# Performance work log

Hardware: AMD Instinct MI355X
Metric: run time of the kernel (lower is better)

## Reference

```python
import jax, jax.numpy as jnp
import numpy as np

N_NODES = 100000
N_EDGES = 3200000
IN_F, HID_F, OUT_F = 128, 64, 32
NEG_SLOPE = 0.2


def setup_inputs() -> dict:
    key = jax.random.key(0)
    ks = jax.random.split(key, 10)
    glorot = lambda k, shape: jax.random.normal(k, shape, jnp.float32) * jnp.sqrt(2.0 / (shape[0] + shape[-1]))
    x = jax.random.normal(ks[0], (N_NODES, IN_F), jnp.float32)
    edge_index = jax.random.randint(ks[1], (2, N_EDGES), 0, N_NODES, jnp.int64)
    return {
        "x": x,
        "edge_index": edge_index,
        "W1": glorot(ks[2], (IN_F, HID_F)),
        "att_src1": glorot(ks[3], (HID_F,)),
        "att_dst1": glorot(ks[4], (HID_F,)),
        "b1": jnp.zeros((HID_F,), jnp.float32),
        "W2": glorot(ks[5], (HID_F, OUT_F)),
        "att_src2": glorot(ks[6], (OUT_F,)),
        "att_dst2": glorot(ks[7], (OUT_F,)),
        "b2": jnp.zeros((OUT_F,), jnp.float32),
    }


def _segment_softmax(logits, seg, num_segments):
    m = jax.ops.segment_max(logits, seg, num_segments=num_segments)
    e = jnp.exp(logits - m[seg])
    s = jax.ops.segment_sum(e, seg, num_segments=num_segments)
    return e / s[seg]


def _gat_conv(x, src, dst, W, a_src, a_dst, b, n):
    h = x @ W                                    # [N, F]
    logits = jax.nn.leaky_relu((h @ a_src)[src] + (h @ a_dst)[dst], NEG_SLOPE)  # [E]
    att = _segment_softmax(logits, dst, n)       # softmax over incoming edges per dst
    out = jax.ops.segment_sum(h[src] * att[:, None], dst, num_segments=n)
    return out + b


def reference(x, edge_index, W1, att_src1, att_dst1, b1, W2, att_src2, att_dst2, b2):
    n = x.shape[0]
    loops = jnp.arange(n, dtype=edge_index.dtype)
    src = jnp.concatenate([edge_index[0], loops])  # PyG GATConv adds self-loops
    dst = jnp.concatenate([edge_index[1], loops])
    h = _gat_conv(x, src, dst, W1, att_src1, att_dst1, b1, n)
    h = jax.nn.relu(h)
    h = _gat_conv(h, src, dst, W2, att_src2, att_dst2, b2, n)
    return jax.nn.softmax(h, axis=1)
```

## Files before the change

### kernel.cpp

```cpp
#include <hip/hip_runtime.h>
#include <hip/hip_fp16.h>

#define N_NODES 100000
#define N_EDGES 3200000
#define ET (N_EDGES + N_NODES)
#define IN_F 128
#define HID_F 64
#define OUT_F 32
#define NEG_SLOPE 0.2f

#define NB 391
#define CHUNK_A 8192
#define BLOCKS_A ((ET + CHUNK_A - 1) / CHUNK_A)
#define BKT_CAP 12288
#define HIST_BLOCKS 400


__global__ __launch_bounds__(256) void histB_kernel(const int* __restrict__ ei,
                                                    int* __restrict__ bpart) {
    __shared__ int lh[NB];
    for (int i = threadIdx.x; i < NB; i += 256) lh[i] = 0;
    __syncthreads();
    int stride = HIST_BLOCKS * 256;
    for (int e = blockIdx.x * 256 + threadIdx.x; e < N_EDGES; e += stride) {
        int dst = ei[N_EDGES + e];
        atomicAdd(&lh[dst >> 8], 1);
    }
    __syncthreads();
    for (int i = threadIdx.x; i < NB; i += 256)
        bpart[blockIdx.x * NB + i] = lh[i];
}


__global__ __launch_bounds__(512) void scanB_kernel(const int* __restrict__ bpart,
                                                    int* __restrict__ bucket_base,
                                                    int* __restrict__ gcursor,
                                                    int* __restrict__ row_ptr) {
    __shared__ int a[NB];
    int t = threadIdx.x;
    int cnt = 0;
    if (t < NB) {
        int v = 0;
        for (int c = 0; c < HIST_BLOCKS; ++c) v += bpart[c * NB + t];
        cnt = v + min(256, N_NODES - (t << 8));
        a[t] = cnt;
    }
    __syncthreads();
    for (int off = 1; off < NB; off <<= 1) {
        int v = 0;
        if (t < NB && t >= off) v = a[t - off];
        __syncthreads();
        if (t < NB) a[t] += v;
        __syncthreads();
    }
    if (t < NB) {
        int base = a[t] - cnt;
        bucket_base[t] = base;
        gcursor[t] = base;
    }
    if (t == 0) { bucket_base[NB] = ET; row_ptr[N_NODES] = ET; }
}


__global__ __launch_bounds__(256) void partA_kernel(const int* __restrict__ ei,
                                                    int* __restrict__ gcursor,
                                                    unsigned* __restrict__ staging) {
    __shared__ int cnt[NB];
    __shared__ int inc[NB];
    __shared__ int delta[NB];
    __shared__ unsigned stg[CHUNK_A];
    __shared__ unsigned short bkt[CHUNK_A];
    int t = threadIdx.x;
    int begin = blockIdx.x * CHUNK_A;
    int n = min(CHUNK_A, ET - begin);

    for (int i = t; i < NB; i += 256) cnt[i] = 0;
    __syncthreads();

    for (int i = t; i < n; i += 256) {
        int e = begin + i;
        int dst = (e < N_EDGES) ? ei[N_EDGES + e] : (e - N_EDGES);
        atomicAdd(&cnt[dst >> 8], 1);
    }
    __syncthreads();

    for (int i = t; i < NB; i += 256) inc[i] = cnt[i];
    __syncthreads();
    for (int off = 1; off < NB; off <<= 1) {
        int i0 = t, i1 = t + 256;
        int v0 = (i0 < NB && i0 >= off) ? inc[i0 - off] : 0;
        int v1 = (i1 < NB && i1 >= off) ? inc[i1 - off] : 0;
        __syncthreads();
        if (i0 < NB) inc[i0] += v0;
        if (i1 < NB) inc[i1] += v1;
        __syncthreads();
    }

    for (int i = t; i < NB; i += 256) {
        int c = cnt[i];
        int ls = inc[i] - c;
        int g = (c > 0) ? atomicAdd(&gcursor[i], c) : 0;
        delta[i] = g - ls;
        cnt[i] = ls;
    }
    __syncthreads();

    for (int i = t; i < n; i += 256) {
        int e = begin + i;
        int src, dst;
        if (e < N_EDGES) { src = ei[e]; dst = ei[N_EDGES + e]; }
        else             { src = dst = e - N_EDGES; }
        int b = dst >> 8;
        int pos = atomicAdd(&cnt[b], 1);
        stg[pos] = ((unsigned)(dst & 255) << 17) | (unsigned)src;
        bkt[pos] = (unsigned short)b;
    }
    __syncthreads();

    for (int i = t; i < n; i += 256) {
        staging[delta[bkt[i]] + i] = stg[i];
    }
}


__global__ __launch_bounds__(256) void partB_kernel(const unsigned* __restrict__ staging,
                                                    const int* __restrict__ bucket_base,
                                                    int* __restrict__ row_ptr,
                                                    int* __restrict__ src_sorted) {
    __shared__ int out_s[BKT_CAP];
    __shared__ int a[256];
    __shared__ int cur[256];
    int b = blockIdx.x, t = threadIdx.x;
    int nb0 = b << 8;
    int nn = min(256, N_NODES - nb0);
    int g0 = bucket_base[b];
    int g1 = bucket_base[b + 1];
    int n = g1 - g0;

    cur[t] = 0;
    __syncthreads();
    for (int i = t; i < n; i += 256)
        atomicAdd(&cur[staging[g0 + i] >> 17], 1);
    __syncthreads();

    int v = cur[t];
    a[t] = v;
    __syncthreads();
    for (int off = 1; off < 256; off <<= 1) {
        int w = (t >= off) ? a[t - off] : 0;
        __syncthreads();
        a[t] += w;
        __syncthreads();
    }
    int pref = a[t] - v;
    cur[t] = pref;
    if (t < nn) row_ptr[nb0 + t] = g0 + pref;
    __syncthreads();

    for (int i = t; i < n; i += 256) {
        unsigned u = staging[g0 + i];
        int pos = atomicAdd(&cur[u >> 17], 1);
        out_s[pos] = (int)(u & 0x1FFFFu);
    }
    __syncthreads();
    for (int i = t; i < n; i += 256)
        src_sorted[g0 + i] = out_s[i];
}


__global__ __launch_bounds__(256) void gemm1_kernel(const float* __restrict__ x,
                                                    const float* __restrict__ W,
                                                    const float* __restrict__ a_src,
                                                    const float* __restrict__ a_dst,
                                                    __half* __restrict__ h,
                                                    float* __restrict__ as,
                                                    float* __restrict__ ad) {
    __shared__ float Wl[IN_F * HID_F];
    __shared__ float Xl[64 * 132];
    int t = threadIdx.x;
    int base = blockIdx.x * 64;

    for (int i = t; i < IN_F * HID_F / 4; i += 256)
        ((float4*)Wl)[i] = ((const float4*)W)[i];
#pragma unroll
    for (int i = 0; i < 8; ++i) {
        int f4 = t + 256 * i;
        int r = f4 >> 5, c4 = f4 & 31;
        int gr = base + r; if (gr >= N_NODES) gr = N_NODES - 1;
        ((float4*)Xl)[r * 33 + c4] = ((const float4*)(x + (size_t)gr * IN_F))[c4];
    }
    __syncthreads();

    int tx = t & 15, ty = t >> 4;
    int col = tx * 4, row0 = ty * 4;

    float4 acc0 = {0,0,0,0}, acc1 = {0,0,0,0}, acc2 = {0,0,0,0}, acc3 = {0,0,0,0};

#pragma unroll 4
    for (int k = 0; k < IN_F; k += 4) {
        float4 xv0 = *(const float4*)&Xl[(row0 + 0) * 132 + k];
        float4 xv1 = *(const float4*)&Xl[(row0 + 1) * 132 + k];
        float4 xv2 = *(const float4*)&Xl[(row0 + 2) * 132 + k];
        float4 xv3 = *(const float4*)&Xl[(row0 + 3) * 132 + k];
        float4 wv0 = *(const float4*)&Wl[(k + 0) * HID_F + col];
        float4 wv1 = *(const float4*)&Wl[(k + 1) * HID_F + col];
        float4 wv2 = *(const float4*)&Wl[(k + 2) * HID_F + col];
        float4 wv3 = *(const float4*)&Wl[(k + 3) * HID_F + col];
#define G1STEP(A, XV) \
        A.x = fmaf(XV.x, wv0.x, A.x); A.y = fmaf(XV.x, wv0.y, A.y); \
        A.z = fmaf(XV.x, wv0.z, A.z); A.w = fmaf(XV.x, wv0.w, A.w); \
        A.x = fmaf(XV.y, wv1.x, A.x); A.y = fmaf(XV.y, wv1.y, A.y); \
        A.z = fmaf(XV.y, wv1.z, A.z); A.w = fmaf(XV.y, wv1.w, A.w); \
        A.x = fmaf(XV.z, wv2.x, A.x); A.y = fmaf(XV.z, wv2.y, A.y); \
        A.z = fmaf(XV.z, wv2.z, A.z); A.w = fmaf(XV.z, wv2.w, A.w); \
        A.x = fmaf(XV.w, wv3.x, A.x); A.y = fmaf(XV.w, wv3.y, A.y); \
        A.z = fmaf(XV.w, wv3.z, A.z); A.w = fmaf(XV.w, wv3.w, A.w);
        G1STEP(acc0, xv0) G1STEP(acc1, xv1) G1STEP(acc2, xv2) G1STEP(acc3, xv3)
#undef G1STEP
    }

    float4 av = *(const float4*)&a_src[col];
    float4 dv = *(const float4*)&a_dst[col];
#define G1OUT(I, A) { \
        int grow = base + row0 + I; \
        float vs = A.x*av.x + A.y*av.y + A.z*av.z + A.w*av.w; \
        float vd = A.x*dv.x + A.y*dv.y + A.z*dv.z + A.w*dv.w; \
        vs += __shfl_xor(vs, 1, 64); vd += __shfl_xor(vd, 1, 64); \
        vs += __shfl_xor(vs, 2, 64); vd += __shfl_xor(vd, 2, 64); \
        vs += __shfl_xor(vs, 4, 64); vd += __shfl_xor(vd, 4, 64); \
        vs += __shfl_xor(vs, 8, 64); vd += __shfl_xor(vd, 8, 64); \
        if (grow < N_NODES) { \
            __half2 p0 = __floats2half2_rn(A.x, A.y); \
            __half2 p1 = __floats2half2_rn(A.z, A.w); \
            __half2* hp = (__half2*)&h[(size_t)grow * HID_F + col]; \
            hp[0] = p0; hp[1] = p1; \
            if (tx == 0) { as[grow] = vs; ad[grow] = vd; } \
        } }
    G1OUT(0, acc0) G1OUT(1, acc1) G1OUT(2, acc2) G1OUT(3, acc3)
#undef G1OUT
}


__global__ __launch_bounds__(256) void agg1_kernel(const __half* __restrict__ h,
                                                   const float* __restrict__ as,
                                                   const float* __restrict__ ad,
                                                   const int* __restrict__ row_ptr,
                                                   const int* __restrict__ src_sorted,
                                                   const float* __restrict__ b,
                                                   float* __restrict__ r1) {
    int n = blockIdx.x * 4 + (threadIdx.x >> 6);
    int lane = threadIdx.x & 63;
    if (n >= N_NODES) return;
    int beg = row_ptr[n], end = row_ptr[n + 1];
    int deg = end - beg;
    float adn = ad[n];

    int e0 = beg + lane;
    int sidx = 0;
    float p = 0.f;
    if (e0 < end) {
        sidx = src_sorted[e0];
        float t = as[sidx] + adn;
        t = (t >= 0.f) ? t : NEG_SLOPE * t;
        p = __expf(t);
    }
    float s = p;

    int g  = lane >> 3;
    int ho = (lane & 7) * 8;

    float4 aL = {0,0,0,0}, aH = {0,0,0,0};
#define ACC1(V, W) { \
        float2 f0 = __half22float2(*(const __half2*)&V.x); \
        float2 f1 = __half22float2(*(const __half2*)&V.y); \
        float2 f2 = __half22float2(*(const __half2*)&V.z); \
        float2 f3 = __half22float2(*(const __half2*)&V.w); \
        aL.x = fmaf(f0.x, W, aL.x); aL.y = fmaf(f0.y, W, aL.y); \
        aL.z = fmaf(f1.x, W, aL.z); aL.w = fmaf(f1.y, W, aL.w); \
        aH.x = fmaf(f2.x, W, aH.x); aH.y = fmaf(f2.y, W, aH.y); \
        aH.z = fmaf(f3.x, W, aH.z); aH.w = fmaf(f3.y, W, aH.w); }

#define BATCH1(K0) { \
        float ws0 = __shfl(p, (K0 + 0) * 8 + g, 64); \
        float ws1 = __shfl(p, (K0 + 1) * 8 + g, 64); \
        float ws2 = __shfl(p, (K0 + 2) * 8 + g, 64); \
        float ws3 = __shfl(p, (K0 + 3) * 8 + g, 64); \
        int   ss0 = __shfl(sidx, (K0 + 0) * 8 + g, 64); \
        int   ss1 = __shfl(sidx, (K0 + 1) * 8 + g, 64); \
        int   ss2 = __shfl(sidx, (K0 + 2) * 8 + g, 64); \
        int   ss3 = __shfl(sidx, (K0 + 3) * 8 + g, 64); \
        uint4 v0 = *(const uint4*)&h[(size_t)ss0 * HID_F + ho]; \
        uint4 v1 = *(const uint4*)&h[(size_t)ss1 * HID_F + ho]; \
        uint4 v2 = *(const uint4*)&h[(size_t)ss2 * HID_F + ho]; \
        uint4 v3 = *(const uint4*)&h[(size_t)ss3 * HID_F + ho]; \
        ACC1(v0, ws0) ACC1(v1, ws1) ACC1(v2, ws2) ACC1(v3, ws3) }

    BATCH1(0)
    if (deg > 32) BATCH1(4)
#undef BATCH1

    for (int cb = beg + 64; cb < end; cb += 64) {
        int e = cb + lane;
        float pr = 0.f;
        int sr = 0;
        if (e < end) {
            sr = src_sorted[e];
            float t = as[sr] + adn;
            t = (t >= 0.f) ? t : NEG_SLOPE * t;
            pr = __expf(t);
            s += pr;
        }
        int cnt = min(64, end - cb);
        int rr = (cnt + 7) >> 3;
        for (int k = 0; k < rr; ++k) {
            float wk = __shfl(pr, k * 8 + g, 64);
            int   sk = __shfl(sr, k * 8 + g, 64);
            uint4 hv = *(const uint4*)&h[(size_t)sk * HID_F + ho];
            ACC1(hv, wk)
        }
    }
#undef ACC1

    s += __shfl_xor(s, 32, 64); s += __shfl_xor(s, 16, 64); s += __shfl_xor(s, 8, 64);
    s += __shfl_xor(s, 4, 64);  s += __shfl_xor(s, 2, 64);  s += __shfl_xor(s, 1, 64);
    float invs = __builtin_amdgcn_rcpf(s);

#define RED1(C) C += __shfl_xor(C, 8, 64); C += __shfl_xor(C, 16, 64); C += __shfl_xor(C, 32, 64);
    RED1(aL.x) RED1(aL.y) RED1(aL.z) RED1(aL.w)
    RED1(aH.x) RED1(aH.y) RED1(aH.z) RED1(aH.w)
#undef RED1

    if (lane < 8) {
        int fo = lane * 8;
        float4 b0 = *(const float4*)&b[fo];
        float4 b1 = *(const float4*)&b[fo + 4];
        float4 vL, vH;
        vL.x = fmaxf(fmaf(aL.x, invs, b0.x), 0.f); vL.y = fmaxf(fmaf(aL.y, invs, b0.y), 0.f);
        vL.z = fmaxf(fmaf(aL.z, invs, b0.z), 0.f); vL.w = fmaxf(fmaf(aL.w, invs, b0.w), 0.f);
        vH.x = fmaxf(fmaf(aH.x, invs, b1.x), 0.f); vH.y = fmaxf(fmaf(aH.y, invs, b1.y), 0.f);
        vH.z = fmaxf(fmaf(aH.z, invs, b1.z), 0.f); vH.w = fmaxf(fmaf(aH.w, invs, b1.w), 0.f);
        *(float4*)&r1[(size_t)n * HID_F + fo] = vL;
        *(float4*)&r1[(size_t)n * HID_F + fo + 4] = vH;
    }
}


__global__ __launch_bounds__(256) void gemm2_kernel(const float* __restrict__ r1,
                                                    const float* __restrict__ W,
                                                    const float* __restrict__ a_src,
                                                    const float* __restrict__ a_dst,
                                                    __half* __restrict__ h2,
                                                    float* __restrict__ as2,
                                                    float* __restrict__ ad2) {
    __shared__ float Wl[HID_F * OUT_F];
    __shared__ float Xl[128 * 68];
    int t = threadIdx.x;
    int base = blockIdx.x * 128;

    for (int i = t; i < HID_F * OUT_F / 4; i += 256)
        ((float4*)Wl)[i] = ((const float4*)W)[i];
#pragma unroll
    for (int i = 0; i < 8; ++i) {
        int f4 = t + 256 * i;
        int r = f4 >> 4, c4 = f4 & 15;
        int gr = base + r; if (gr >= N_NODES) gr = N_NODES - 1;
        ((float4*)Xl)[r * 17 + c4] = ((const float4*)(r1 + (size_t)gr * HID_F))[c4];
    }
    __syncthreads();

    int tx = t & 7, ty = t >> 3;
    int col = tx * 4, row0 = ty * 4;

    float4 acc0 = {0,0,0,0}, acc1 = {0,0,0,0}, acc2 = {0,0,0,0}, acc3 = {0,0,0,0};

#pragma unroll 4
    for (int k = 0; k < HID_F; k += 4) {
        float4 xv0 = *(const float4*)&Xl[(row0 + 0) * 68 + k];
        float4 xv1 = *(const float4*)&Xl[(row0 + 1) * 68 + k];
        float4 xv2 = *(const float4*)&Xl[(row0 + 2) * 68 + k];
        float4 xv3 = *(const float4*)&Xl[(row0 + 3) * 68 + k];
        float4 wv0 = *(const float4*)&Wl[(k + 0) * OUT_F + col];
        float4 wv1 = *(const float4*)&Wl[(k + 1) * OUT_F + col];
        float4 wv2 = *(const float4*)&Wl[(k + 2) * OUT_F + col];
        float4 wv3 = *(const float4*)&Wl[(k + 3) * OUT_F + col];
#define G2STEP(A, XV) \
        A.x = fmaf(XV.x, wv0.x, A.x); A.y = fmaf(XV.x, wv0.y, A.y); \
        A.z = fmaf(XV.x, wv0.z, A.z); A.w = fmaf(XV.x, wv0.w, A.w); \
        A.x = fmaf(XV.y, wv1.x, A.x); A.y = fmaf(XV.y, wv1.y, A.y); \
        A.z = fmaf(XV.y, wv1.z, A.z); A.w = fmaf(XV.y, wv1.w, A.w); \
        A.x = fmaf(XV.z, wv2.x, A.x); A.y = fmaf(XV.z, wv2.y, A.y); \
        A.z = fmaf(XV.z, wv2.z, A.z); A.w = fmaf(XV.z, wv2.w, A.w); \
        A.x = fmaf(XV.w, wv3.x, A.x); A.y = fmaf(XV.w, wv3.y, A.y); \
        A.z = fmaf(XV.w, wv3.z, A.z); A.w = fmaf(XV.w, wv3.w, A.w);
        G2STEP(acc0, xv0) G2STEP(acc1, xv1) G2STEP(acc2, xv2) G2STEP(acc3, xv3)
#undef G2STEP
    }

    float4 av = *(const float4*)&a_src[col];
    float4 dv = *(const float4*)&a_dst[col];
#define G2OUT(I, A) { \
        int grow = base + row0 + I; \
        float vs = A.x*av.x + A.y*av.y + A.z*av.z + A.w*av.w; \
        float vd = A.x*dv.x + A.y*dv.y + A.z*dv.z + A.w*dv.w; \
        vs += __shfl_xor(vs, 1, 64); vd += __shfl_xor(vd, 1, 64); \
        vs += __shfl_xor(vs, 2, 64); vd += __shfl_xor(vd, 2, 64); \
        vs += __shfl_xor(vs, 4, 64); vd += __shfl_xor(vd, 4, 64); \
        if (grow < N_NODES) { \
            __half2 p0 = __floats2half2_rn(A.x, A.y); \
            __half2 p1 = __floats2half2_rn(A.z, A.w); \
            __half2* hp = (__half2*)&h2[(size_t)grow * OUT_F + col]; \
            hp[0] = p0; hp[1] = p1; \
            if (tx == 0) { as2[grow] = vs; ad2[grow] = vd; } \
        } }
    G2OUT(0, acc0) G2OUT(1, acc1) G2OUT(2, acc2) G2OUT(3, acc3)
#undef G2OUT
}


__global__ __launch_bounds__(256) void agg2_kernel(const __half* __restrict__ h2,
                                                   const float* __restrict__ as2,
                                                   const float* __restrict__ ad2,
                                                   const int* __restrict__ row_ptr,
                                                   const int* __restrict__ src_sorted,
                                                   const float* __restrict__ b2,
                                                   float* __restrict__ out) {
    int n = blockIdx.x * 4 + (threadIdx.x >> 6);
    int lane = threadIdx.x & 63;
    if (n >= N_NODES) return;
    int beg = row_ptr[n], end = row_ptr[n + 1];
    int deg = end - beg;
    float adn = ad2[n];

    int e0 = beg + lane;
    int sidx = 0;
    float p = 0.f;
    if (e0 < end) {
        sidx = src_sorted[e0];
        float t = as2[sidx] + adn;
        t = (t >= 0.f) ? t : NEG_SLOPE * t;
        p = __expf(t);
    }
    float s = p;

    int g  = lane >> 3;
    int ho = (lane & 7) * 4;

    float4 acc = {0.f, 0.f, 0.f, 0.f};
#define ACC2(V, W) { \
        float2 f0 = __half22float2(*(const __half2*)&V.x); \
        float2 f1 = __half22float2(*(const __half2*)&V.y); \
        acc.x = fmaf(f0.x, W, acc.x); acc.y = fmaf(f0.y, W, acc.y); \
        acc.z = fmaf(f1.x, W, acc.z); acc.w = fmaf(f1.y, W, acc.w); }

#define BATCH2(K0) { \
        float ws0 = __shfl(p, (K0 + 0) * 8 + g, 64); \
        float ws1 = __shfl(p, (K0 + 1) * 8 + g, 64); \
        float ws2 = __shfl(p, (K0 + 2) * 8 + g, 64); \
        float ws3 = __shfl(p, (K0 + 3) * 8 + g, 64); \
        int   ss0 = __shfl(sidx, (K0 + 0) * 8 + g, 64); \
        int   ss1 = __shfl(sidx, (K0 + 1) * 8 + g, 64); \
        int   ss2 = __shfl(sidx, (K0 + 2) * 8 + g, 64); \
        int   ss3 = __shfl(sidx, (K0 + 3) * 8 + g, 64); \
        uint2 v0 = *(const uint2*)&h2[(size_t)ss0 * OUT_F + ho]; \
        uint2 v1 = *(const uint2*)&h2[(size_t)ss1 * OUT_F + ho]; \
        uint2 v2 = *(const uint2*)&h2[(size_t)ss2 * OUT_F + ho]; \
        uint2 v3 = *(const uint2*)&h2[(size_t)ss3 * OUT_F + ho]; \
        ACC2(v0, ws0) ACC2(v1, ws1) ACC2(v2, ws2) ACC2(v3, ws3) }

    BATCH2(0)
    if (deg > 32) BATCH2(4)
#undef BATCH2

    for (int cb = beg + 64; cb < end; cb += 64) {
        int e = cb + lane;
        float pr = 0.f;
        int sr = 0;
        if (e < end) {
            sr = src_sorted[e];
            float t = as2[sr] + adn;
            t = (t >= 0.f) ? t : NEG_SLOPE * t;
            pr = __expf(t);
            s += pr;
        }
        int cnt = min(64, end - cb);
        int rr = (cnt + 7) >> 3;
        for (int k = 0; k < rr; ++k) {
            float wk = __shfl(pr, k * 8 + g, 64);
            int   sk = __shfl(sr, k * 8 + g, 64);
            uint2 hv = *(const uint2*)&h2[(size_t)sk * OUT_F + ho];
            ACC2(hv, wk)
        }
    }
#undef ACC2

    s += __shfl_xor(s, 32, 64); s += __shfl_xor(s, 16, 64); s += __shfl_xor(s, 8, 64);
    s += __shfl_xor(s, 4, 64);  s += __shfl_xor(s, 2, 64);  s += __shfl_xor(s, 1, 64);
    float invs = __builtin_amdgcn_rcpf(s);

    acc.x += __shfl_xor(acc.x, 8, 64); acc.x += __shfl_xor(acc.x, 16, 64); acc.x += __shfl_xor(acc.x, 32, 64);
    acc.y += __shfl_xor(acc.y, 8, 64); acc.y += __shfl_xor(acc.y, 16, 64); acc.y += __shfl_xor(acc.y, 32, 64);
    acc.z += __shfl_xor(acc.z, 8, 64); acc.z += __shfl_xor(acc.z, 16, 64); acc.z += __shfl_xor(acc.z, 32, 64);
    acc.w += __shfl_xor(acc.w, 8, 64); acc.w += __shfl_xor(acc.w, 16, 64); acc.w += __shfl_xor(acc.w, 32, 64);

    int fo = (lane & 7) * 4;
    float4 bv = *(const float4*)&b2[fo];
    float4 v;
    v.x = fmaf(acc.x, invs, bv.x); v.y = fmaf(acc.y, invs, bv.y);
    v.z = fmaf(acc.z, invs, bv.z); v.w = fmaf(acc.w, invs, bv.w);

    float4 ev;
    ev.x = __expf(v.x); ev.y = __expf(v.y);
    ev.z = __expf(v.z); ev.w = __expf(v.w);
    float ls = ev.x + ev.y + ev.z + ev.w;
    ls += __shfl_xor(ls, 1, 64);
    ls += __shfl_xor(ls, 2, 64);
    ls += __shfl_xor(ls, 4, 64);
    float invl = __builtin_amdgcn_rcpf(ls);
    if (lane < 8) {
        float4 o;
        o.x = ev.x * invl; o.y = ev.y * invl; o.z = ev.z * invl; o.w = ev.w * invl;
        *(float4*)&out[(size_t)n * OUT_F + fo] = o;
    }
}


extern "C" void kernel_launch(void* const* d_in, const int* in_sizes, int n_in,
                              void* d_out, int out_size, void* d_ws, size_t ws_size,
                              hipStream_t stream) {
    const float* x     = (const float*)d_in[0];
    const int*   ei    = (const int*)d_in[1];
    const float* W1    = (const float*)d_in[2];
    const float* asrc1 = (const float*)d_in[3];
    const float* adst1 = (const float*)d_in[4];
    const float* b1    = (const float*)d_in[5];
    const float* W2    = (const float*)d_in[6];
    const float* asrc2 = (const float*)d_in[7];
    const float* adst2 = (const float*)d_in[8];
    const float* b2    = (const float*)d_in[9];
    float* out = (float*)d_out;

    char* p = (char*)d_ws;
    auto alloc = [&](size_t bytes) {
        char* q = p;
        p += (bytes + 255) & ~size_t(255);
        return q;
    };
    int*    row_ptr     = (int*)   alloc(sizeof(int) * (N_NODES + 1));
    int*    bpart       = (int*)   alloc(sizeof(int) * (size_t)HIST_BLOCKS * NB);
    int*    bucket_base = (int*)   alloc(sizeof(int) * (NB + 1));
    int*    gcursor     = (int*)   alloc(sizeof(int) * NB);
    int*    src_sorted  = (int*)   alloc(sizeof(int) * (size_t)ET);
    __half* h1          = (__half*)alloc(sizeof(__half) * (size_t)N_NODES * HID_F);
    float*  as1         = (float*) alloc(sizeof(float) * N_NODES);
    float*  ad1         = (float*) alloc(sizeof(float) * N_NODES);
    float*  r1          = (float*) alloc(sizeof(float) * (size_t)N_NODES * HID_F);
    __half* h2          = (__half*)alloc(sizeof(__half) * (size_t)N_NODES * OUT_F);
    float*  as2v        = (float*) alloc(sizeof(float) * N_NODES);
    float*  ad2v        = (float*) alloc(sizeof(float) * N_NODES);
    unsigned* staging   = (unsigned*)r1;

    hipLaunchKernelGGL(histB_kernel, dim3(HIST_BLOCKS), dim3(256), 0, stream, ei, bpart);
    hipLaunchKernelGGL(scanB_kernel, dim3(1), dim3(512), 0, stream,
                       bpart, bucket_base, gcursor, row_ptr);
    hipLaunchKernelGGL(partA_kernel, dim3(BLOCKS_A), dim3(256), 0, stream, ei, gcursor, staging);
    hipLaunchKernelGGL(partB_kernel, dim3(NB), dim3(256), 0, stream,
                       staging, bucket_base, row_ptr, src_sorted);
    hipLaunchKernelGGL(gemm1_kernel, dim3((N_NODES + 63) / 64), dim3(256), 0, stream,
                       x, W1, asrc1, adst1, h1, as1, ad1);
    hipLaunchKernelGGL(agg1_kernel, dim3((N_NODES + 3) / 4), dim3(256), 0, stream,
                       h1, as1, ad1, row_ptr, src_sorted, b1, r1);
    hipLaunchKernelGGL(gemm2_kernel, dim3((N_NODES + 127) / 128), dim3(256), 0, stream,
                       r1, W2, asrc2, adst2, h2, as2v, ad2v);
    hipLaunchKernelGGL(agg2_kernel, dim3((N_NODES + 3) / 4), dim3(256), 0, stream,
                       h2, as2v, ad2v, row_ptr, src_sorted, b2, out);
}
```

Before: 233.3 us.

## Use fma_mix for half accumulation, unconditional 8-way gather, halve chunk size

Replaces the half-to-float conversions plus FMAs in both aggregation kernels with inline v_fma_mix_f32 instructions that read the packed fp16 operand directly. The first 64-edge batch now always issues all 8 gathers up front, instead of doing 4 and a conditional 4 more, to raise memory-level parallelism. Gather indexing switches from size_t to unsigned math, and CHUNK_A is halved so the bucketing stage launches more blocks. In exchange, low-degree nodes pay for redundant loads of row 0 and register pressure rises.

```diff
diff --git a/kernel.cpp b/kernel.cpp
--- a/kernel.cpp
+++ b/kernel.cpp
@@ -10,10 +10,17 @@
 #define NEG_SLOPE 0.2f
 
 #define NB 391
-#define CHUNK_A 8192
+#define CHUNK_A 4096
 #define BLOCKS_A ((ET + CHUNK_A - 1) / CHUNK_A)
 #define BKT_CAP 12288
 #define HIST_BLOCKS 400
+
+#define FMAMIX_LO(ACC, PK, W) \
+    asm("v_fma_mix_f32 %0, %1, %2, %0 op_sel:[0,0,0] op_sel_hi:[1,0,0]" \
+        : "+v"(ACC) : "v"(PK), "v"(W))
+#define FMAMIX_HI(ACC, PK, W) \
+    asm("v_fma_mix_f32 %0, %1, %2, %0 op_sel:[1,0,0] op_sel_hi:[1,0,0]" \
+        : "+v"(ACC) : "v"(PK), "v"(W))
 
 
 __global__ __launch_bounds__(256) void histB_kernel(const int* __restrict__ ei,
@@ -252,7 +259,6 @@
     int lane = threadIdx.x & 63;
     if (n >= N_NODES) return;
     int beg = row_ptr[n], end = row_ptr[n + 1];
-    int deg = end - beg;
     float adn = ad[n];
 
     int e0 = beg + lane;
@@ -271,33 +277,23 @@
 
     float4 aL = {0,0,0,0}, aH = {0,0,0,0};
 #define ACC1(V, W) { \
-        float2 f0 = __half22float2(*(const __half2*)&V.x); \
-        float2 f1 = __half22float2(*(const __half2*)&V.y); \
-        float2 f2 = __half22float2(*(const __half2*)&V.z); \
-        float2 f3 = __half22float2(*(const __half2*)&V.w); \
-        aL.x = fmaf(f0.x, W, aL.x); aL.y = fmaf(f0.y, W, aL.y); \
-        aL.z = fmaf(f1.x, W, aL.z); aL.w = fmaf(f1.y, W, aL.w); \
-        aH.x = fmaf(f2.x, W, aH.x); aH.y = fmaf(f2.y, W, aH.y); \
-        aH.z = fmaf(f3.x, W, aH.z); aH.w = fmaf(f3.y, W, aH.w); }
-
-#define BATCH1(K0) { \
-        float ws0 = __shfl(p, (K0 + 0) * 8 + g, 64); \
-        float ws1 = __shfl(p, (K0 + 1) * 8 + g, 64); \
-        float ws2 = __shfl(p, (K0 + 2) * 8 + g, 64); \
-        float ws3 = __shfl(p, (K0 + 3) * 8 + g, 64); \
-        int   ss0 = __shfl(sidx, (K0 + 0) * 8 + g, 64); \
-        int   ss1 = __shfl(sidx, (K0 + 1) * 8 + g, 64); \
-        int   ss2 = __shfl(sidx, (K0 + 2) * 8 + g, 64); \
-        int   ss3 = __shfl(sidx, (K0 + 3) * 8 + g, 64); \
-        uint4 v0 = *(const uint4*)&h[(size_t)ss0 * HID_F + ho]; \
-        uint4 v1 = *(const uint4*)&h[(size_t)ss1 * HID_F + ho]; \
-        uint4 v2 = *(const uint4*)&h[(size_t)ss2 * HID_F + ho]; \
-        uint4 v3 = *(const uint4*)&h[(size_t)ss3 * HID_F + ho]; \
-        ACC1(v0, ws0) ACC1(v1, ws1) ACC1(v2, ws2) ACC1(v3, ws3) }
-
-    BATCH1(0)
-    if (deg > 32) BATCH1(4)
-#undef BATCH1
+        FMAMIX_LO(aL.x, V.x, W); FMAMIX_HI(aL.y, V.x, W); \
+        FMAMIX_LO(aL.z, V.y, W); FMAMIX_HI(aL.w, V.y, W); \
+        FMAMIX_LO(aH.x, V.z, W); FMAMIX_HI(aH.y, V.z, W); \
+        FMAMIX_LO(aH.z, V.w, W); FMAMIX_HI(aH.w, V.w, W); }
+
+    float ws[8]; int ss[8];
+#pragma unroll
+    for (int k = 0; k < 8; ++k) {
+        ws[k] = __shfl(p,    k * 8 + g, 64);
+        ss[k] = __shfl(sidx, k * 8 + g, 64);
+    }
+    uint4 vv[8];
+#pragma unroll
+    for (int k = 0; k < 8; ++k)
+        vv[k] = *(const uint4*)&h[(unsigned)ss[k] * HID_F + ho];
+#pragma unroll
+    for (int k = 0; k < 8; ++k) ACC1(vv[k], ws[k])
 
     for (int cb = beg + 64; cb < end; cb += 64) {
         int e = cb + lane;
@@ -315,7 +311,7 @@
         for (int k = 0; k < rr; ++k) {
             float wk = __shfl(pr, k * 8 + g, 64);
             int   sk = __shfl(sr, k * 8 + g, 64);
-            uint4 hv = *(const uint4*)&h[(size_t)sk * HID_F + ho];
+            uint4 hv = *(const uint4*)&h[(unsigned)sk * HID_F + ho];
             ACC1(hv, wk)
         }
     }
@@ -428,7 +424,6 @@
     int lane = threadIdx.x & 63;
     if (n >= N_NODES) return;
     int beg = row_ptr[n], end = row_ptr[n + 1];
-    int deg = end - beg;
     float adn = ad2[n];
 
     int e0 = beg + lane;
@@ -447,29 +442,21 @@
 
     float4 acc = {0.f, 0.f, 0.f, 0.f};
 #define ACC2(V, W) { \
-        float2 f0 = __half22float2(*(const __half2*)&V.x); \
-        float2 f1 = __half22float2(*(const __half2*)&V.y); \
-        acc.x = fmaf(f0.x, W, acc.x); acc.y = fmaf(f0.y, W, acc.y); \
-        acc.z = fmaf(f1.x, W, acc.z); acc.w = fmaf(f1.y, W, acc.w); }
-
-#define BATCH2(K0) { \
-        float ws0 = __shfl(p, (K0 + 0) * 8 + g, 64); \
-        float ws1 = __shfl(p, (K0 + 1) * 8 + g, 64); \
-        float ws2 = __shfl(p, (K0 + 2) * 8 + g, 64); \
-        float ws3 = __shfl(p, (K0 + 3) * 8 + g, 64); \
-        int   ss0 = __shfl(sidx, (K0 + 0) * 8 + g, 64); \
-        int   ss1 = __shfl(sidx, (K0 + 1) * 8 + g, 64); \
-        int   ss2 = __shfl(sidx, (K0 + 2) * 8 + g, 64); \
-        int   ss3 = __shfl(sidx, (K0 + 3) * 8 + g, 64); \
-        uint2 v0 = *(const uint2*)&h2[(size_t)ss0 * OUT_F + ho]; \
-        uint2 v1 = *(const uint2*)&h2[(size_t)ss1 * OUT_F + ho]; \
-        uint2 v2 = *(const uint2*)&h2[(size_t)ss2 * OUT_F + ho]; \
-        uint2 v3 = *(const uint2*)&h2[(size_t)ss3 * OUT_F + ho]; \
-        ACC2(v0, ws0) ACC2(v1, ws1) ACC2(v2, ws2) ACC2(v3, ws3) }
-
-    BATCH2(0)
-    if (deg > 32) BATCH2(4)
-#undef BATCH2
+        FMAMIX_LO(acc.x, V.x, W); FMAMIX_HI(acc.y, V.x, W); \
+        FMAMIX_LO(acc.z, V.y, W); FMAMIX_HI(acc.w, V.y, W); }
+
+    float ws[8]; int ss[8];
+#pragma unroll
+    for (int k = 0; k < 8; ++k) {
+        ws[k] = __shfl(p,    k * 8 + g, 64);
+        ss[k] = __shfl(sidx, k * 8 + g, 64);
+    }
+    uint2 q[8];
+#pragma unroll
+    for (int k = 0; k < 8; ++k)
+        q[k] = *(const uint2*)&h2[(unsigned)ss[k] * OUT_F + ho];
+#pragma unroll
+    for (int k = 0; k < 8; ++k) ACC2(q[k], ws[k])
 
     for (int cb = beg + 64; cb < end; cb += 64) {
         int e = cb + lane;
@@ -487,7 +474,7 @@
         for (int k = 0; k < rr; ++k) {
             float wk = __shfl(pr, k * 8 + g, 64);
             int   sk = __shfl(sr, k * 8 + g, 64);
-            uint2 hv = *(const uint2*)&h2[(size_t)sk * OUT_F + ho];
+            uint2 hv = *(const uint2*)&h2[(unsigned)sk * OUT_F + ho];
             ACC2(hv, wk)
         }
     }
```

New measurement: 240.7 us. 3.2% more time.
